# Performance work log

Measured on AMD Instinct MI355X. Metric: run time of the kernel, lower is better.

The kernel has to match this reference:

```python
import jax, jax.numpy as jnp
import numpy as np

C = 768           # input_embed_dim
G = 16            # conv groups
CG = C // G       # channels per group (48)
MAX_TOKENS = 64
N = 65536         # sequence / spatial length
B = 1             # .item() in the torch code forces batch == 1
EPS = 1e-5


def _layernorm(x, gamma, beta):
    mu = jnp.mean(x, axis=-1, keepdims=True)
    var = jnp.mean((x - mu) ** 2, axis=-1, keepdims=True)
    return (x - mu) * jax.lax.rsqrt(var + EPS) * gamma + beta


def _grouped_pointwise(x, w):
    # x: [B, N, C]; w: [G, CG_out, CG_in] (torch Conv2d weight [C, CG, 1, 1] regrouped)
    xg = x.reshape(x.shape[0], x.shape[1], G, CG)           # [B, N, G, CG]
    yg = jnp.einsum('bngi,goi->bngo', xg, w)                 # [B, N, G, CG]
    return yg.reshape(x.shape[0], x.shape[1], C)


def setup_inputs() -> dict:
    key = jax.random.key(0)
    ks = jax.random.split(key, 9)
    s = 1.0 / np.sqrt(CG)
    inp = {
        'x': jax.random.normal(ks[0], (B, N, C), dtype=jnp.float32),
        'tn_gamma': jnp.ones((C,), jnp.float32),
        'tn_beta': jnp.zeros((C,), jnp.float32),
        'w1': jax.random.uniform(ks[1], (G, CG, CG), jnp.float32, -s, s),   # grouped conv 1
        'w2': jax.random.uniform(ks[2], (MAX_TOKENS, C), jnp.float32, -1 / np.sqrt(C), 1 / np.sqrt(C)),  # pointwise conv C->MAX_TOKENS
        'wf': jax.random.uniform(ks[3], (G, CG, CG), jnp.float32, -s, s),   # grouped feat conv
        'pred_w': jax.random.uniform(ks[4], (C,), jnp.float32, -1 / np.sqrt(C), 1 / np.sqrt(C)),
        'pred_b': jax.random.uniform(ks[5], (1,), jnp.float32, -1 / np.sqrt(C), 1 / np.sqrt(C)),
        'n_gamma': jnp.ones((C,), jnp.float32),
        'n_beta': jnp.zeros((C,), jnp.float32),
    }
    return inp


def reference(x, tn_gamma, tn_beta, w1, w2, wf, pred_w, pred_b, n_gamma, n_beta):
    # LayerNorm over channels
    xn = _layernorm(x, tn_gamma, tn_beta)                    # [B, N, C]

    # token_predictor: AdaptiveAvgPool2d over (N,1) -> Linear(C,1) -> Sigmoid
    pooled = jnp.mean(xn, axis=1)                            # [B, C]
    ratio = jax.nn.sigmoid(pooled @ pred_w + pred_b[0])      # [B]
    # num_tokens = int(ratio.item() * MAX_TOKENS)  (truncation == floor, ratio > 0)
    num_tokens = jnp.floor(ratio[0] * MAX_TOKENS).astype(jnp.int32)
    tok_mask = (jnp.arange(MAX_TOKENS) < num_tokens)[None, :, None]  # [1, T, 1]

    # tokenLearner: grouped 1x1 conv -> ReLU -> pointwise conv C -> MAX_TOKENS
    h = jax.nn.relu(_grouped_pointwise(xn, w1))              # [B, N, C]
    scores = jnp.einsum('bnc,tc->btn', h, w2)                # [B, T, N]
    # softmax is per-token-row over N, so slicing rows before/after softmax is equivalent;
    # we mask dropped rows to zero (fixed output shape instead of dynamic slice).
    selected = jax.nn.softmax(scores, axis=-1)
    selected = jnp.where(tok_mask, selected, 0.0)            # [B, T, N]

    feat = _grouped_pointwise(xn, wf)                        # [B, N, C]
    out = jnp.einsum('btn,bnc->btc', selected, feat)         # [B, T, C]
    out = _layernorm(out, n_gamma, n_beta)
    out = jnp.where(tok_mask, out, 0.0)                      # zero rows beyond num_tokens
    return selected, out
```

## Files before the change

### kernel.cpp

```cpp
#include <hip/hip_runtime.h>
#include <hip/hip_bf16.h>

#define DEV __device__ __forceinline__

constexpr int N = 65536;
constexpr int C = 768;
constexpr int T = 64;

using bf16 = __hip_bfloat16;
using short8 = __attribute__((ext_vector_type(8))) short;
using f32x4  = __attribute__((ext_vector_type(4))) float;

DEV ushort f2bits(float v) { union { __hip_bfloat16 h; ushort u; } x; x.h = __float2bfloat16(v); return x.u; }
DEV float bits2f(ushort b) { union { uint u; float f; } x; x.u = ((uint)b) << 16; return x.f; }
DEV f32x4 mfma16(short8 a, short8 b, f32x4 c) { return __builtin_amdgcn_mfma_f32_16x16x32_bf16(a, b, c, 0, 0, 0); }
DEV int swz(int row, int col) { return row * 64 + (col ^ ((row & 7) << 3)); }

DEV float wredsum(float v) {
#pragma unroll
  for (int o = 32; o > 0; o >>= 1) v += __shfl_xor(v, o, 64);
  return v;
}

__global__ __launch_bounds__(256) void k_wprep(const float* __restrict__ w1,
                                               const float* __restrict__ w2,
                                               const float* __restrict__ wf,
                                               short* __restrict__ w1p,
                                               short* __restrict__ w2p,
                                               short* __restrict__ wfp) {
  const int b = blockIdx.x, tid = threadIdx.x;
  if (b < 192) {
    int idx = b * 256 + tid;
    int j = idx & 7, lane = (idx >> 3) & 63, u = idx >> 9;
    int kt = u & 1, v = u >> 1, ot = v % 3, g = v / 3;
    int o = ot * 16 + (lane & 15), k = kt * 32 + ((lane >> 4) & 3) * 8 + j;
    w1p[idx] = (k < 48) ? (short)f2bits(w1[g * 2304 + o * 48 + k]) : (short)0;
  } else if (b < 448) {
    int idx = (b - 192) * 256 + tid;
    int j = idx & 7, lane = (idx >> 3) & 63, u = idx >> 9;
    int kt = u & 1, v = u >> 1, tt = v & 3, g = v >> 2;
    int t = tt * 16 + (lane & 15), k = kt * 32 + ((lane >> 4) & 3) * 8 + j;
    w2p[idx] = (k < 48) ? (short)f2bits(w2[t * 768 + g * 48 + k]) : (short)0;
  } else {
    int idx = (b - 448) * 256 + tid;
    int j = idx & 7, lane = (idx >> 3) & 63, u = idx >> 9;
    int kt = u & 1, v = u >> 1, ot = v % 3, g = v / 3;
    int o = ot * 16 + (lane & 15), k = kt * 32 + ((lane >> 4) & 3) * 8 + j;
    wfp[idx] = (k < 48) ? (short)f2bits(wf[g * 2304 + o * 48 + k]) : (short)0;
  }
}

__global__ __launch_bounds__(256, 4) void k_ln(const float4* __restrict__ x,
                                               const float4* __restrict__ gam,
                                               const float4* __restrict__ bet,
                                               uint2* __restrict__ xn,
                                               float* __restrict__ pooled) {
  const int tid = threadIdx.x, wave = tid >> 6, lane = tid & 63;
  float4 gg[3], bb[3], pool[3];
#pragma unroll
  for (int j = 0; j < 3; j++) {
    gg[j] = gam[lane + 64 * j]; bb[j] = bet[lane + 64 * j];
    pool[j] = make_float4(0.f, 0.f, 0.f, 0.f);
  }
  const int r0 = (blockIdx.x * 4 + wave) * 16;
  for (int r = r0; r < r0 + 16; ++r) {
    const float4* xr = x + (size_t)r * 192;
    float4 v[3]; float s = 0.f, q = 0.f;
#pragma unroll
    for (int j = 0; j < 3; j++) {
      v[j] = xr[lane + 64 * j];
      s += v[j].x + v[j].y + v[j].z + v[j].w;
      q += v[j].x * v[j].x + v[j].y * v[j].y + v[j].z * v[j].z + v[j].w * v[j].w;
    }
    s = wredsum(s); q = wredsum(q);
    const float mu = s * (1.f / C);
    const float rs = rsqrtf(q * (1.f / C) - mu * mu + 1e-5f);
    uint2* xo = xn + (size_t)r * 192;
#pragma unroll
    for (int j = 0; j < 3; j++) {
      float y0 = (v[j].x - mu) * rs * gg[j].x + bb[j].x;
      float y1 = (v[j].y - mu) * rs * gg[j].y + bb[j].y;
      float y2 = (v[j].z - mu) * rs * gg[j].z + bb[j].z;
      float y3 = (v[j].w - mu) * rs * gg[j].w + bb[j].w;
      pool[j].x += y0; pool[j].y += y1; pool[j].z += y2; pool[j].w += y3;
      xo[lane + 64 * j] = make_uint2((uint)f2bits(y0) | ((uint)f2bits(y1) << 16),
                                     (uint)f2bits(y2) | ((uint)f2bits(y3) << 16));
    }
  }
  __shared__ float lp[4][C];
#pragma unroll
  for (int j = 0; j < 3; j++) {
    int base = (lane + 64 * j) * 4;
    lp[wave][base] = pool[j].x; lp[wave][base + 1] = pool[j].y;
    lp[wave][base + 2] = pool[j].z; lp[wave][base + 3] = pool[j].w;
  }
  __syncthreads();
  for (int c = tid; c < C; c += 256)
    atomicAdd(&pooled[c], lp[0][c] + lp[1][c] + lp[2][c] + lp[3][c]);
}

__global__ __launch_bounds__(256) void k_pool(const float* __restrict__ pooled,
                                              const float* __restrict__ pw,
                                              const float* __restrict__ pb,
                                              int* __restrict__ ntok) {
  const int tid = threadIdx.x, wave = tid >> 6, lane = tid & 63;
  float a = 0.f;
  for (int c = tid; c < C; c += 256) a += pooled[c] * (1.f / N) * pw[c];
  a = wredsum(a);
  __shared__ float red[4];
  if (lane == 0) red[wave] = a;
  __syncthreads();
  if (tid == 0) {
    float d = red[0] + red[1] + red[2] + red[3] + pb[0];
    float ratio = 1.f / (1.f + expf(-d));
    int nt = (int)floorf(ratio * 64.f);
    nt = nt < 0 ? 0 : (nt > 64 ? 64 : nt);
    *ntok = nt;
  }
}

__global__ __launch_bounds__(256, 4) void k_cs(const short* __restrict__ xn,
                                               const short* __restrict__ w1p,
                                               const short* __restrict__ w2p,
                                               float* __restrict__ scores) {
  __shared__ __align__(16) short hs[4][2][16 * 64];
  const int tid = threadIdx.x, wave = tid >> 6, lane = tid & 63;
  const int l15 = lane & 15, g2 = lane >> 4;
  {
    uint* hz = (uint*)hs[wave];
    for (int i = lane; i < 1024; i += 64) hz[i] = 0u;
  }
  const int row0 = blockIdx.x * 64 + wave * 16;
  f32x4 acc[4];
#pragma unroll
  for (int t = 0; t < 4; ++t) acc[t] = (f32x4){0.f, 0.f, 0.f, 0.f};
  const short* xrow = xn + (size_t)(row0 + l15) * 768;
  const int lo8 = lane * 8;

  short8 bx0 = *(const short8*)(xrow + g2 * 8);
  short8 bx1 = *(const short8*)(xrow + 32 + g2 * 8);
#pragma unroll 2
  for (int g = 0; g < 16; ++g) {
    const int gn = (g < 15) ? g + 1 : 15;
    short8 nbx0 = *(const short8*)(xrow + gn * 48 + g2 * 8);
    short8 nbx1 = *(const short8*)(xrow + gn * 48 + 32 + g2 * 8);
    short* hw = hs[wave][g & 1];
    const short* w1g = w1p + g * 3072;
#pragma unroll
    for (int ot = 0; ot < 3; ++ot) {
      short8 a0 = *(const short8*)(w1g + (ot * 2 + 0) * 512 + lo8);
      short8 a1 = *(const short8*)(w1g + (ot * 2 + 1) * 512 + lo8);
      f32x4 h = (f32x4){0.f, 0.f, 0.f, 0.f};
      h = mfma16(a0, bx0, h);
      h = mfma16(a1, bx1, h);
      uint lo = (uint)f2bits(fmaxf(h[0], 0.f)) | ((uint)f2bits(fmaxf(h[1], 0.f)) << 16);
      uint hi = (uint)f2bits(fmaxf(h[2], 0.f)) | ((uint)f2bits(fmaxf(h[3], 0.f)) << 16);
      *(uint2*)&hw[swz(l15, ot * 16 + g2 * 4)] = make_uint2(lo, hi);
    }
    short8 hb0 = *(const short8*)&hw[swz(l15, g2 * 8)];
    short8 hb1 = *(const short8*)&hw[swz(l15, 32 + g2 * 8)];
    const short* w2g = w2p + g * 4096;
#pragma unroll
    for (int tt = 0; tt < 4; ++tt) {
      short8 a0 = *(const short8*)(w2g + (tt * 2 + 0) * 512 + lo8);
      short8 a1 = *(const short8*)(w2g + (tt * 2 + 1) * 512 + lo8);
      acc[tt] = mfma16(a0, hb0, acc[tt]);
      acc[tt] = mfma16(a1, hb1, acc[tt]);
    }
    bx0 = nbx0; bx1 = nbx1;
  }
#pragma unroll
  for (int tt = 0; tt < 4; ++tt)
#pragma unroll
    for (int r = 0; r < 4; ++r)
      scores[(size_t)(tt * 16 + g2 * 4 + r) * N + row0 + l15] = acc[tt][r];
}

__global__ __launch_bounds__(256) void k_stats(const float* __restrict__ scores,
                                               float2* __restrict__ part) {
  const int t = blockIdx.x >> 3, s = blockIdx.x & 7;
  const float* row = scores + (size_t)t * N + s * 8192;
  float m = -1e30f, l = 0.f;
  for (int i = threadIdx.x; i < 8192; i += 256) {
    float v = row[i];
    if (v > m) { l = l * __expf(m - v) + 1.f; m = v; }
    else       { l += __expf(v - m); }
  }
#pragma unroll
  for (int o = 32; o > 0; o >>= 1) {
    float m2 = __shfl_xor(m, o, 64), l2 = __shfl_xor(l, o, 64);
    float M = fmaxf(m, m2);
    l = l * __expf(m - M) + l2 * __expf(m2 - M); m = M;
  }
  __shared__ float sm[4], sl[4];
  const int wave = threadIdx.x >> 6, lane = threadIdx.x & 63;
  if (lane == 0) { sm[wave] = m; sl[wave] = l; }
  __syncthreads();
  if (threadIdx.x == 0) {
    float M = sm[0], L = sl[0];
    for (int w = 1; w < 4; w++) { float M2 = fmaxf(M, sm[w]); L = L * __expf(M - M2) + sl[w] * __expf(sm[w] - M2); M = M2; }
    part[blockIdx.x] = make_float2(M, L);
  }
}

__global__ __launch_bounds__(256) void k_sel(const float* __restrict__ scores,
                                             const float2* __restrict__ part,
                                             const int* __restrict__ ntokp,
                                             float* __restrict__ sel,
                                             ushort* __restrict__ selb) {
  const int t = blockIdx.x >> 3, s = blockIdx.x & 7;
  float M = -1e30f, L = 0.f;
#pragma unroll
  for (int i = 0; i < 8; i++) {
    float2 p = part[t * 8 + i];
    float M2 = fmaxf(M, p.x);
    L = L * __expf(M - M2) + p.y * __expf(p.x - M2); M = M2;
  }
  const float li = 1.f / L;
  const bool on = t < *ntokp;
  const size_t base = (size_t)t * N + s * 8192;
  const float4* sp = (const float4*)(scores + base);
  float4* op = (float4*)(sel + base);
  uint2* ob = (uint2*)(selb + base);
#pragma unroll
  for (int it = 0; it < 8; ++it) {
    int idx = threadIdx.x + 256 * it;
    float4 v = sp[idx];
    float4 e;
    e.x = on ? __expf(v.x - M) * li : 0.f;
    e.y = on ? __expf(v.y - M) * li : 0.f;
    e.z = on ? __expf(v.z - M) * li : 0.f;
    e.w = on ? __expf(v.w - M) * li : 0.f;
    op[idx] = e;
    ob[idx] = make_uint2((uint)f2bits(e.x) | ((uint)f2bits(e.y) << 16),
                         (uint)f2bits(e.z) | ((uint)f2bits(e.w) << 16));
  }
}

__global__ __launch_bounds__(512, 2) void k_og(const short* __restrict__ xn,
                                               const short* __restrict__ wfp,
                                               const short* __restrict__ selb,
                                               const int* __restrict__ ntokp,
                                               ushort* __restrict__ out_part) {
  __shared__ __align__(16) short ft[2][192 * 64];
  const int tid = threadIdx.x, wave = tid >> 6, lane = tid & 63;
  const int l15 = lane & 15, g2 = lane >> 4;
  const int cb = blockIdx.y, nb = blockIdx.x;
  const int ntok = *ntokp;
  const int gq = wave >> 1, ntq = wave & 1;
  const int tt = wave >> 1, chalf = wave & 1;
  const bool act = (tt * 16) < ntok;
  short8 wb0[3], wb1[3];
  {
    const short* wb = wfp + (size_t)(cb * 4 + gq) * 3072 + lane * 8;
#pragma unroll
    for (int ot = 0; ot < 3; ++ot) {
      wb0[ot] = *(const short8*)(wb + (ot * 2 + 0) * 512);
      wb1[ot] = *(const short8*)(wb + (ot * 2 + 1) * 512);
    }
  }
  f32x4 acc[6];
#pragma unroll
  for (int k = 0; k < 6; ++k) acc[k] = (f32x4){0.f, 0.f, 0.f, 0.f};

  const short* xr0 = xn + (size_t)(nb * 512 + ntq * 16 + l15) * 768 + (cb * 4 + gq) * 48;
  const short* sr0 = selb + (size_t)(tt * 16 + l15) * N + nb * 512 + g2 * 8;

  short8 bx0 = *(const short8*)(xr0 + g2 * 8);
  short8 bx1 = *(const short8*)(xr0 + 32 + g2 * 8);
  short8 ps = {};
  short8 nx0 = bx0, nx1 = bx1, nps = ps;

  for (int ns = 0; ns <= 16; ++ns) {
    if (ns < 16) {
      const int nsn = (ns < 15) ? ns + 1 : 15;
      nx0 = *(const short8*)(xr0 + nsn * 24576 + g2 * 8);
      nx1 = *(const short8*)(xr0 + nsn * 24576 + 32 + g2 * 8);
      nps = *(const short8*)(sr0 + ns * 32);
      short* f = ft[ns & 1];
#pragma unroll
      for (int ot = 0; ot < 3; ++ot) {
        f32x4 d = (f32x4){0.f, 0.f, 0.f, 0.f};
        d = mfma16(bx0, wb0[ot], d);
        d = mfma16(bx1, wb1[ot], d);
        int c = gq * 48 + ot * 16 + l15;
        uint lo = (uint)f2bits(d[0]) | ((uint)f2bits(d[1]) << 16);
        uint hi = (uint)f2bits(d[2]) | ((uint)f2bits(d[3]) << 16);
        *(uint2*)&f[c * 64 + ((ntq * 16 + g2 * 4) ^ ((c & 7) << 3))] = make_uint2(lo, hi);
      }
    }
    if (ns >= 1 && act) {
      const short* f = ft[(ns - 1) & 1];
#pragma unroll
      for (int ct = 0; ct < 6; ++ct) {
        int c = (chalf * 6 + ct) * 16 + l15;
        short8 fb = *(const short8*)&f[c * 64 + ((g2 * 8) ^ ((c & 7) << 3))];
        acc[ct] = mfma16(ps, fb, acc[ct]);
      }
    }
    __syncthreads();
    bx0 = nx0; bx1 = nx1; ps = nps;
  }
#pragma unroll
  for (int ct = 0; ct < 6; ++ct)
#pragma unroll
    for (int r = 0; r < 4; ++r) {
      int t = tt * 16 + g2 * 4 + r;
      int c = cb * 192 + (chalf * 6 + ct) * 16 + l15;
      out_part[(size_t)nb * (64 * 768) + t * 768 + c] = f2bits(acc[ct][r]);
    }
}

__global__ __launch_bounds__(192) void k_fin(const ushort* __restrict__ out_part,
                                             const float* __restrict__ ng,
                                             const float* __restrict__ nb_,
                                             const int* __restrict__ ntokp,
                                             float* __restrict__ outp) {
  const int t = blockIdx.x, tid = threadIdx.x;
  const int wave = tid >> 6, lane = tid & 63;
  const int c4 = tid * 4;
  float4 s = make_float4(0.f, 0.f, 0.f, 0.f);
  const ushort* base = out_part + t * 768 + c4;
  for (int nbk = 0; nbk < 128; ++nbk) {
    uint2 v = *(const uint2*)(base + (size_t)nbk * 49152);
    s.x += bits2f((ushort)(v.x & 0xffff)); s.y += bits2f((ushort)(v.x >> 16));
    s.z += bits2f((ushort)(v.y & 0xffff)); s.w += bits2f((ushort)(v.y >> 16));
  }
  float ss = s.x + s.y + s.z + s.w;
  float qq = s.x * s.x + s.y * s.y + s.z * s.z + s.w * s.w;
  ss = wredsum(ss); qq = wredsum(qq);
  __shared__ float sm[3], sq[3];
  if (lane == 0) { sm[wave] = ss; sq[wave] = qq; }
  __syncthreads();
  const float S = sm[0] + sm[1] + sm[2], Q = sq[0] + sq[1] + sq[2];
  const float mu = S * (1.f / C);
  const float rs = rsqrtf(Q * (1.f / C) - mu * mu + 1e-5f);
  const bool on = t < *ntokp;
  float4 g = *(const float4*)(ng + c4), b = *(const float4*)(nb_ + c4);
  float4 y;
  y.x = on ? (s.x - mu) * rs * g.x + b.x : 0.f;
  y.y = on ? (s.y - mu) * rs * g.y + b.y : 0.f;
  y.z = on ? (s.z - mu) * rs * g.z + b.z : 0.f;
  y.w = on ? (s.w - mu) * rs * g.w + b.w : 0.f;
  *(float4*)(outp + t * 768 + c4) = y;
}

extern "C" void kernel_launch(void* const* d_in, const int* in_sizes, int n_in,
                              void* d_out, int out_size, void* d_ws, size_t ws_size,
                              hipStream_t stream) {
  const float* x  = (const float*)d_in[0];
  const float* tg = (const float*)d_in[1];
  const float* tb = (const float*)d_in[2];
  const float* w1 = (const float*)d_in[3];
  const float* w2 = (const float*)d_in[4];
  const float* wf = (const float*)d_in[5];
  const float* pw = (const float*)d_in[6];
  const float* pb = (const float*)d_in[7];
  const float* ng = (const float*)d_in[8];
  const float* nb = (const float*)d_in[9];

  char* ws = (char*)d_ws;
  float*  pooled = (float*)(ws + 0);
  float2* part   = (float2*)(ws + 4096);
  int*    ntok   = (int*)(ws + 8704);
  short*  w1p    = (short*)(ws + 16384);
  short*  w2p    = (short*)(ws + 114688);
  short*  wfp    = (short*)(ws + 245760);
  short*  xn     = (short*)(ws + 344064);
  float*  scores = (float*)(ws + 101007360);
  ushort* opart  = (ushort*)(ws + 101007360);
  ushort* selb   = (ushort*)(ws + 117784576);

  float* sel  = (float*)d_out;
  float* outp = (float*)d_out + (size_t)T * N;

  (void)hipMemsetAsync(pooled, 0, C * sizeof(float), stream);

  k_wprep <<<640, 256, 0, stream>>>(w1, w2, wf, w1p, w2p, wfp);
  k_ln    <<<1024, 256, 0, stream>>>((const float4*)x, (const float4*)tg, (const float4*)tb,
                                     (uint2*)xn, pooled);
  k_pool  <<<1, 256, 0, stream>>>(pooled, pw, pb, ntok);
  k_cs    <<<1024, 256, 0, stream>>>(xn, w1p, w2p, scores);
  k_stats <<<512, 256, 0, stream>>>(scores, part);
  k_sel   <<<512, 256, 0, stream>>>(scores, part, ntok, sel, selb);
  k_og    <<<dim3(128, 4), 512, 0, stream>>>(xn, wfp, (const short*)selb, ntok, opart);
  k_fin   <<<64, 192, 0, stream>>>(opart, ng, nb, ntok, outp);
}
```

Baseline: 438.4 us.

## Fuse softmax stats into score GEMM and normalization into output GEMM

```diff
diff --git a/kernel.cpp b/kernel.cpp
--- a/kernel.cpp
+++ b/kernel.cpp
@@ -122,8 +122,10 @@
 __global__ __launch_bounds__(256, 4) void k_cs(const short* __restrict__ xn,
                                                const short* __restrict__ w1p,
                                                const short* __restrict__ w2p,
-                                               float* __restrict__ scores) {
+                                               float* __restrict__ scores,
+                                               float2* __restrict__ part2) {
   __shared__ __align__(16) short hs[4][2][16 * 64];
+  __shared__ float2 stats[4][64];
   const int tid = threadIdx.x, wave = tid >> 6, lane = tid & 63;
   const int l15 = lane & 15, g2 = lane >> 4;
   {
@@ -174,73 +176,69 @@
 #pragma unroll
     for (int r = 0; r < 4; ++r)
       scores[(size_t)(tt * 16 + g2 * 4 + r) * N + row0 + l15] = acc[tt][r];
-}
-
-__global__ __launch_bounds__(256) void k_stats(const float* __restrict__ scores,
-                                               float2* __restrict__ part) {
-  const int t = blockIdx.x >> 3, s = blockIdx.x & 7;
-  const float* row = scores + (size_t)t * N + s * 8192;
-  float m = -1e30f, l = 0.f;
-  for (int i = threadIdx.x; i < 8192; i += 256) {
-    float v = row[i];
-    if (v > m) { l = l * __expf(m - v) + 1.f; m = v; }
-    else       { l += __expf(v - m); }
+
+#pragma unroll
+  for (int tt = 0; tt < 4; ++tt) {
+#pragma unroll
+    for (int r = 0; r < 4; ++r) {
+      float v = acc[tt][r];
+      float m = v;
+#pragma unroll
+      for (int o = 1; o < 16; o <<= 1) m = fmaxf(m, __shfl_xor(m, o, 64));
+      float l = __expf(v - m);
+#pragma unroll
+      for (int o = 1; o < 16; o <<= 1) l += __shfl_xor(l, o, 64);
+      if (l15 == 0) stats[wave][tt * 16 + g2 * 4 + r] = make_float2(m, l);
+    }
+  }
+  __syncthreads();
+  if (tid < 64) {
+    float2 a = stats[0][tid], b = stats[1][tid];
+    float M1 = fmaxf(a.x, b.x), L1 = a.y * __expf(a.x - M1) + b.y * __expf(b.x - M1);
+    float2 c = stats[2][tid], d = stats[3][tid];
+    float M2 = fmaxf(c.x, d.x), L2 = c.y * __expf(c.x - M2) + d.y * __expf(d.x - M2);
+    float M = fmaxf(M1, M2), L = L1 * __expf(M1 - M) + L2 * __expf(M2 - M);
+    part2[(size_t)tid * 1024 + blockIdx.x] = make_float2(M, L);
+  }
+}
+
+__global__ __launch_bounds__(256) void k_merge(const float2* __restrict__ part2,
+                                               float* __restrict__ Mv,
+                                               float* __restrict__ Li) {
+  const int t = blockIdx.x, tid = threadIdx.x;
+  float M = -1e30f, L = 0.f;
+  for (int i = tid; i < 1024; i += 256) {
+    float2 p = part2[(size_t)t * 1024 + i];
+    float Mx = fmaxf(M, p.x);
+    L = L * __expf(M - Mx) + p.y * __expf(p.x - Mx); M = Mx;
   }
 #pragma unroll
   for (int o = 32; o > 0; o >>= 1) {
-    float m2 = __shfl_xor(m, o, 64), l2 = __shfl_xor(l, o, 64);
-    float M = fmaxf(m, m2);
-    l = l * __expf(m - M) + l2 * __expf(m2 - M); m = M;
+    float m2 = __shfl_xor(M, o, 64), l2 = __shfl_xor(L, o, 64);
+    float Mx = fmaxf(M, m2);
+    L = L * __expf(M - Mx) + l2 * __expf(m2 - Mx); M = Mx;
   }
   __shared__ float sm[4], sl[4];
-  const int wave = threadIdx.x >> 6, lane = threadIdx.x & 63;
-  if (lane == 0) { sm[wave] = m; sl[wave] = l; }
+  const int wave = tid >> 6, lane = tid & 63;
+  if (lane == 0) { sm[wave] = M; sl[wave] = L; }
   __syncthreads();
-  if (threadIdx.x == 0) {
-    float M = sm[0], L = sl[0];
-    for (int w = 1; w < 4; w++) { float M2 = fmaxf(M, sm[w]); L = L * __expf(M - M2) + sl[w] * __expf(sm[w] - M2); M = M2; }
-    part[blockIdx.x] = make_float2(M, L);
-  }
-}
-
-__global__ __launch_bounds__(256) void k_sel(const float* __restrict__ scores,
-                                             const float2* __restrict__ part,
-                                             const int* __restrict__ ntokp,
-                                             float* __restrict__ sel,
-                                             ushort* __restrict__ selb) {
-  const int t = blockIdx.x >> 3, s = blockIdx.x & 7;
-  float M = -1e30f, L = 0.f;
-#pragma unroll
-  for (int i = 0; i < 8; i++) {
-    float2 p = part[t * 8 + i];
-    float M2 = fmaxf(M, p.x);
-    L = L * __expf(M - M2) + p.y * __expf(p.x - M2); M = M2;
-  }
-  const float li = 1.f / L;
-  const bool on = t < *ntokp;
-  const size_t base = (size_t)t * N + s * 8192;
-  const float4* sp = (const float4*)(scores + base);
-  float4* op = (float4*)(sel + base);
-  uint2* ob = (uint2*)(selb + base);
-#pragma unroll
-  for (int it = 0; it < 8; ++it) {
-    int idx = threadIdx.x + 256 * it;
-    float4 v = sp[idx];
-    float4 e;
-    e.x = on ? __expf(v.x - M) * li : 0.f;
-    e.y = on ? __expf(v.y - M) * li : 0.f;
-    e.z = on ? __expf(v.z - M) * li : 0.f;
-    e.w = on ? __expf(v.w - M) * li : 0.f;
-    op[idx] = e;
-    ob[idx] = make_uint2((uint)f2bits(e.x) | ((uint)f2bits(e.y) << 16),
-                         (uint)f2bits(e.z) | ((uint)f2bits(e.w) << 16));
-  }
-}
-
-__global__ __launch_bounds__(512, 2) void k_og(const short* __restrict__ xn,
+  if (tid == 0) {
+    float Mm = sm[0], Ll = sl[0];
+    for (int w = 1; w < 4; w++) {
+      float Mx = fmaxf(Mm, sm[w]);
+      Ll = Ll * __expf(Mm - Mx) + sl[w] * __expf(sm[w] - Mx); Mm = Mx;
+    }
+    Mv[t] = Mm; Li[t] = 1.f / Ll;
+  }
+}
+
+__global__ __launch_bounds__(512, 4) void k_og(const short* __restrict__ xn,
                                                const short* __restrict__ wfp,
-                                               const short* __restrict__ selb,
+                                               const float* __restrict__ scores,
+                                               const float* __restrict__ Mv,
+                                               const float* __restrict__ Li,
                                                const int* __restrict__ ntokp,
+                                               float* __restrict__ sel,
                                                ushort* __restrict__ out_part) {
   __shared__ __align__(16) short ft[2][192 * 64];
   const int tid = threadIdx.x, wave = tid >> 6, lane = tid & 63;
@@ -250,6 +248,9 @@
   const int gq = wave >> 1, ntq = wave & 1;
   const int tt = wave >> 1, chalf = wave & 1;
   const bool act = (tt * 16) < ntok;
+  const int tmy = tt * 16 + l15;
+  const bool on = tmy < ntok;
+  const float M = Mv[tmy], LI = Li[tmy];
   short8 wb0[3], wb1[3];
   {
     const short* wb = wfp + (size_t)(cb * 4 + gq) * 3072 + lane * 8;
@@ -264,7 +265,8 @@
   for (int k = 0; k < 6; ++k) acc[k] = (f32x4){0.f, 0.f, 0.f, 0.f};
 
   const short* xr0 = xn + (size_t)(nb * 512 + ntq * 16 + l15) * 768 + (cb * 4 + gq) * 48;
-  const short* sr0 = selb + (size_t)(tt * 16 + l15) * N + nb * 512 + g2 * 8;
+  const float* sr0 = scores + (size_t)tmy * N + nb * 512 + g2 * 8;
+  float* so0 = sel + (size_t)tmy * N + nb * 512 + g2 * 8;
 
   short8 bx0 = *(const short8*)(xr0 + g2 * 8);
   short8 bx1 = *(const short8*)(xr0 + 32 + g2 * 8);
@@ -276,7 +278,25 @@
       const int nsn = (ns < 15) ? ns + 1 : 15;
       nx0 = *(const short8*)(xr0 + nsn * 24576 + g2 * 8);
       nx1 = *(const short8*)(xr0 + nsn * 24576 + 32 + g2 * 8);
-      nps = *(const short8*)(sr0 + ns * 32);
+      float4 s0 = *(const float4*)(sr0 + ns * 32);
+      float4 s1 = *(const float4*)(sr0 + ns * 32 + 4);
+      float4 e0, e1;
+      e0.x = on ? __expf(s0.x - M) * LI : 0.f;
+      e0.y = on ? __expf(s0.y - M) * LI : 0.f;
+      e0.z = on ? __expf(s0.z - M) * LI : 0.f;
+      e0.w = on ? __expf(s0.w - M) * LI : 0.f;
+      e1.x = on ? __expf(s1.x - M) * LI : 0.f;
+      e1.y = on ? __expf(s1.y - M) * LI : 0.f;
+      e1.z = on ? __expf(s1.z - M) * LI : 0.f;
+      e1.w = on ? __expf(s1.w - M) * LI : 0.f;
+      if (chalf == 0) {
+        *(float4*)(so0 + ns * 32) = e0;
+        *(float4*)(so0 + ns * 32 + 4) = e1;
+      }
+      nps[0] = (short)f2bits(e0.x); nps[1] = (short)f2bits(e0.y);
+      nps[2] = (short)f2bits(e0.z); nps[3] = (short)f2bits(e0.w);
+      nps[4] = (short)f2bits(e1.x); nps[5] = (short)f2bits(e1.y);
+      nps[6] = (short)f2bits(e1.z); nps[7] = (short)f2bits(e1.w);
       short* f = ft[ns & 1];
 #pragma unroll
       for (int ot = 0; ot < 3; ++ot) {
@@ -361,15 +381,16 @@
 
   char* ws = (char*)d_ws;
   float*  pooled = (float*)(ws + 0);
-  float2* part   = (float2*)(ws + 4096);
   int*    ntok   = (int*)(ws + 8704);
+  float*  Mv     = (float*)(ws + 8960);
+  float*  Li     = (float*)(ws + 9216);
   short*  w1p    = (short*)(ws + 16384);
   short*  w2p    = (short*)(ws + 114688);
   short*  wfp    = (short*)(ws + 245760);
-  short*  xn     = (short*)(ws + 344064);
-  float*  scores = (float*)(ws + 101007360);
-  ushort* opart  = (ushort*)(ws + 101007360);
-  ushort* selb   = (ushort*)(ws + 117784576);
+  float2* part2  = (float2*)(ws + 344064);
+  short*  xn     = (short*)(ws + 868352);
+  float*  scores = (float*)(ws + 101531648);
+  ushort* opart  = (ushort*)(ws + 118308864);
 
   float* sel  = (float*)d_out;
   float* outp = (float*)d_out + (size_t)T * N;
@@ -380,9 +401,8 @@
   k_ln    <<<1024, 256, 0, stream>>>((const float4*)x, (const float4*)tg, (const float4*)tb,
                                      (uint2*)xn, pooled);
   k_pool  <<<1, 256, 0, stream>>>(pooled, pw, pb, ntok);
-  k_cs    <<<1024, 256, 0, stream>>>(xn, w1p, w2p, scores);
-  k_stats <<<512, 256, 0, stream>>>(scores, part);
-  k_sel   <<<512, 256, 0, stream>>>(scores, part, ntok, sel, selb);
-  k_og    <<<dim3(128, 4), 512, 0, stream>>>(xn, wfp, (const short*)selb, ntok, opart);
+  k_cs    <<<1024, 256, 0, stream>>>(xn, w1p, w2p, scores, part2);
+  k_merge <<<64, 256, 0, stream>>>(part2, Mv, Li);
+  k_og    <<<dim3(128, 4), 512, 0, stream>>>(xn, wfp, scores, Mv, Li, ntok, sel, opart);
   k_fin   <<<64, 192, 0, stream>>>(opart, ng, nb, ntok, outp);
 }
```

Measured after the change: 445.9 us. About the same (+1.7%).
